# Kernel tuning notes

Hardware: AMD Instinct MI355X
Metric: run time of the kernel (lower is better)

The kernel has to match this reference:

```python
import jax, jax.numpy as jnp
import numpy as np


def setup_inputs() -> dict:
    key = jax.random.key(0)
    kx, ke = jax.random.split(key)
    N, T, D, M = 64, 400, 1024, 256
    x = jax.random.normal(kx, (N, T, D), dtype=jnp.float32)
    embedding = jax.random.normal(ke, (M, D), dtype=jnp.float32)
    return {"x": x, "embedding": embedding}


def reference(x, embedding):
    # x: (N, T, D); embedding (codebook): (M, D)
    M, D = embedding.shape
    # L2_distance: normalize codebook rows, distances to detached x
    emb_norm = embedding / (jnp.linalg.norm(embedding, axis=1, keepdims=True) + 1e-4)
    x_flat = jax.lax.stop_gradient(x).reshape(-1, D)  # (N*T, D)
    distances = (jnp.sum(emb_norm ** 2, axis=1)[None, :]
                 + jnp.sum(x_flat ** 2, axis=1, keepdims=True)
                 - 2.0 * (x_flat @ emb_norm.T))  # (N*T, M)
    indices = jnp.argmin(distances, axis=-1)  # (N*T,)
    encodings = jax.nn.one_hot(indices, M, dtype=jnp.float32)  # (N*T, M)
    quantized = embedding[indices].reshape(x.shape)  # gather from UNnormalized codebook

    # commitment loss (both sides detached in original -> constant)
    commitment_loss = jnp.mean(
        (jax.lax.stop_gradient(x) - jax.lax.stop_gradient(quantized)) ** 2)

    # straight-through + average with quantized
    quantized_st = x + jax.lax.stop_gradient(quantized - x)
    quantized_ = (quantized_st + quantized) / 2.0

    avg_probs = jnp.mean(encodings, axis=0)  # (M,)
    perplexity = jnp.exp(-jnp.sum(avg_probs * jnp.log(avg_probs + 1e-10)))
    return quantized_, commitment_loss, perplexity
```

## Files before the change

### kernel.cpp

```cpp
#include <hip/hip_runtime.h>
#include <cstdint>
#include <cstddef>


typedef __attribute__((ext_vector_type(8))) short short8;
typedef __attribute__((ext_vector_type(4))) float f32x4;

namespace {
constexpr int kNT = 25600;
constexpr int kD  = 1024;
constexpr int kM  = 256;
constexpr size_t kQElems = (size_t)kNT * kD;

constexpr int WS_IMG_H = 0;
constexpr int WS_IMG_L = 131072;
constexpr int WS_E2N   = 262144;
constexpr int WS_SCL   = WS_E2N + kM;
constexpr int WS_E2R   = WS_SCL + kM;
constexpr int WS_COM   = WS_E2R + kM;
constexpr int WS_HIST  = WS_COM + 4;
constexpr int WS_ZERO_BYTES = (WS_HIST + kM - WS_COM) * 4;
}

typedef __attribute__((address_space(3))) unsigned int        lds_u32;
typedef const __attribute__((address_space(1))) unsigned int  glb_u32;
typedef const __attribute__((address_space(3))) char          lds_chc;

__device__ __forceinline__ void gl2lds16(const void* g, void* l) {
  __builtin_amdgcn_global_load_lds((glb_u32*)g, (lds_u32*)l, 16, 0, 0);
}

template <int OFF>
__device__ __forceinline__ short8 ldsr(lds_chc* p) {
  short8 r;
  asm volatile("ds_read_b128 %0, %1 offset:%c2" : "=v"(r) : "v"(p), "i"(OFF));
  return r;
}
template <int OFF>
__device__ __forceinline__ void ldsw(lds_chc* p, short8 v) {
  asm volatile("ds_write_b128 %0, %1 offset:%c2" :: "v"(p), "v"(v), "i"(OFF) : "memory");
}
__device__ __forceinline__ f32x4 gld4(const float* p) {
  f32x4 r;
  asm volatile("global_load_dwordx4 %0, %1, off" : "=v"(r) : "v"(p));
  return r;
}

__global__ __launch_bounds__(256) void vq_normalize(const float* __restrict__ emb,
                                                    float* __restrict__ ws) {
  const int m = blockIdx.x;
  const int t = threadIdx.x;
  const float4 v = reinterpret_cast<const float4*>(emb + (size_t)m * kD)[t];
  float s = v.x * v.x + v.y * v.y + v.z * v.z + v.w * v.w;
#pragma unroll
  for (int mask = 32; mask >= 1; mask >>= 1) s += __shfl_xor(s, mask);
  __shared__ float red[4];
  if ((t & 63) == 0) red[t >> 6] = s;
  __syncthreads();
  const float tot = red[0] + red[1] + red[2] + red[3];
  const float sc  = sqrtf(tot) + 1e-4f;
  const float inv = 1.0f / sc;
  const float4 nv = make_float4(v.x * inv, v.y * inv, v.z * inv, v.w * inv);

  float s2 = nv.x * nv.x + nv.y * nv.y + nv.z * nv.z + nv.w * nv.w;
#pragma unroll
  for (int mask = 32; mask >= 1; mask >>= 1) s2 += __shfl_xor(s2, mask);
  __syncthreads();
  if ((t & 63) == 0) red[t >> 6] = s2;
  __syncthreads();
  if (t == 0) {
    ws[WS_E2N + m] = red[0] + red[1] + red[2] + red[3];
    ws[WS_SCL + m] = sc;
    ws[WS_E2R + m] = tot;
  }

  unsigned short* imgh = (unsigned short*)(ws + WS_IMG_H);
  unsigned short* imgl = (unsigned short*)(ws + WS_IMG_L);
  const int c  = t >> 3;
  const int g  = (t >> 1) & 3;
  const int sq = g ^ ((m >> 1) & 3);
  const int base = c * 8192 + m * 32 + sq * 8 + 4 * (t & 1);
  ushort4 hq, lq;
#pragma unroll
  for (int j = 0; j < 4; ++j) {
    const float fv = (&nv.x)[j];
    const unsigned int b = __float_as_uint(fv);
    const unsigned short hi = (unsigned short)(b >> 16);
    const float lof = fv - __uint_as_float(b & 0xFFFF0000u);
    const unsigned short lo = (unsigned short)(__float_as_uint(lof) >> 16);
    (&hq.x)[j] = hi; (&lq.x)[j] = lo;
  }
  *(ushort4*)(imgh + base) = hq;
  *(ushort4*)(imgl + base) = lq;
}


#define DMASTAGE(KCN)                                                          \
  {                                                                            \
    const unsigned short* gh_ = imgH + ((size_t)(KCN) << 13) + (w << 11) + (l << 3); \
    const unsigned short* gl_ = imgL + ((size_t)(KCN) << 13) + (w << 11) + (l << 3); \
    gl2lds16(gh_,        BslU);                                                \
    gl2lds16(gh_ +  512, BslU + 1024);                                         \
    gl2lds16(gh_ + 1024, BslU + 2048);                                         \
    gl2lds16(gh_ + 1536, BslU + 3072);                                         \
    gl2lds16(gl_,        BslU + 4096);                                         \
    gl2lds16(gl_ +  512, BslU + 5120);                                         \
    gl2lds16(gl_ + 1024, BslU + 6144);                                         \
    gl2lds16(gl_ + 1536, BslU + 7168);                                         \
  }

#define CONV8(F0, F1, AH, AL)                                                  \
  {                                                                            \
    union { short8 v; unsigned short u[8]; } H_, L_;                           \
    _Pragma("unroll")                                                          \
    for (int jj_ = 0; jj_ < 8; ++jj_) {                                        \
      const float fv_ = (jj_ < 4) ? (F0)[jj_] : (F1)[jj_ - 4];                 \
      const unsigned int b_ = __float_as_uint(fv_);                            \
      H_.u[jj_] = (unsigned short)(b_ >> 16);                                  \
      const float lo_ = fv_ - __uint_as_float(b_ & 0xFFFF0000u);               \
      L_.u[jj_] = (unsigned short)(__float_as_uint(lo_) >> 16);                \
      x2 += fv_ * fv_;                                                         \
    }                                                                          \
    AH = H_.v; AL = L_.v;                                                      \
  }

#define MMQ(AR, B0, B1, B2, B3, RT)                                                        \
  acc[RT][0] = __builtin_amdgcn_mfma_f32_16x16x32_bf16(AR, B0, acc[RT][0], 0, 0, 0);       \
  acc[RT][1] = __builtin_amdgcn_mfma_f32_16x16x32_bf16(AR, B1, acc[RT][1], 0, 0, 0);       \
  acc[RT][2] = __builtin_amdgcn_mfma_f32_16x16x32_bf16(AR, B2, acc[RT][2], 0, 0, 0);       \
  acc[RT][3] = __builtin_amdgcn_mfma_f32_16x16x32_bf16(AR, B3, acc[RT][3], 0, 0, 0);
#define MMPASS(A0, A1, A2, A3, B0, B1, B2, B3)                                 \
  MMQ(A0, B0, B1, B2, B3, 0) MMQ(A1, B0, B1, B2, B3, 1)                        \
  MMQ(A2, B0, B1, B2, B3, 2) MMQ(A3, B0, B1, B2, B3, 3)

#define VQ_ITER5(KC, XB, XC0, XC1, XN0, XN1)                                   \
  {                                                                            \
    asm volatile("s_waitcnt vmcnt(2)" ::: "memory");          \
    __builtin_amdgcn_sched_barrier(0);                                         \
    short8 a0h, a1h, a2h, a3h, a0l, a1l, a2l, a3l;                             \
    short8 b0h, b1h, b2h, b3h, b0l, b1l, b2l, b3l;                             \
    a0h = ldsr<32768 + (XB) * 8192 + 0 * 1024>(pA);                            \
    a1h = ldsr<32768 + (XB) * 8192 + 1 * 1024>(pA);                            \
    a2h = ldsr<32768 + (XB) * 8192 + 2 * 1024>(pA);                            \
    a3h = ldsr<32768 + (XB) * 8192 + 3 * 1024>(pA);                            \
    a0l = ldsr<32768 + (XB) * 8192 + 4096 + 0 * 1024>(pA);                     \
    a1l = ldsr<32768 + (XB) * 8192 + 4096 + 1 * 1024>(pA);                     \
    a2l = ldsr<32768 + (XB) * 8192 + 4096 + 2 * 1024>(pA);                     \
    a3l = ldsr<32768 + (XB) * 8192 + 4096 + 3 * 1024>(pA);                     \
    b0h = ldsr<0 * 1024>(pB);                                                  \
    b1h = ldsr<1 * 1024>(pB);                                                  \
    b2h = ldsr<2 * 1024>(pB);                                                  \
    b3h = ldsr<3 * 1024>(pB);                                                  \
    b0l = ldsr<4096 + 0 * 1024>(pB);                                           \
    b1l = ldsr<4096 + 1 * 1024>(pB);                                           \
    b2l = ldsr<4096 + 2 * 1024>(pB);                                           \
    b3l = ldsr<4096 + 3 * 1024>(pB);                                           \
    asm volatile("s_waitcnt lgkmcnt(0)" ::: "memory");      \
    __builtin_amdgcn_sched_barrier(0);                                         \
    {                      \
      const int kcn_ = ((KC) + 1 < 32) ? (KC) + 1 : 31;                        \
      DMASTAGE(kcn_)                                                           \
    }                                                                          \
    {                                                                          \
      const int kc2_ = ((KC) + 2 < 32) ? (KC) + 2 : 31;                        \
      XN0 = gld4(xrow + kc2_ * 32);                                            \
      XN1 = gld4(xrow + kc2_ * 32 + 4);                                        \
    }                                                                          \
    __builtin_amdgcn_s_setprio(1);                                             \
    MMPASS(a0h, a1h, a2h, a3h, b0h, b1h, b2h, b3h)                  \
    MMPASS(a0h, a1h, a2h, a3h, b0l, b1l, b2l, b3l)                  \
    __builtin_amdgcn_s_setprio(0);                                             \
    asm volatile("s_waitcnt vmcnt(10)" ::: "memory");       \
    __builtin_amdgcn_sched_barrier(0);                                         \
    if ((KC) < 31) {                                                           \
      short8 cah, cal;                                                         \
      CONV8(XC0, XC1, cah, cal)                                                \
      ldsw<32768 + ((XB) ^ 1) * 8192 + 0>(pW, cah);                            \
      ldsw<32768 + ((XB) ^ 1) * 8192 + 4096>(pW, cal);                         \
    }                                                                          \
    __builtin_amdgcn_s_setprio(1);                                             \
    MMPASS(a0l, a1l, a2l, a3l, b0h, b1h, b2h, b3h)                  \
    __builtin_amdgcn_s_setprio(0);                                             \
    asm volatile("s_waitcnt lgkmcnt(0)" ::: "memory");      \
    __builtin_amdgcn_s_barrier();                                              \
  }

__global__ __launch_bounds__(256, 2) void vq_main(const float* __restrict__ x,
                                                  const float* __restrict__ emb,
                                                  const float* __restrict__ wsc,
                                                  float* __restrict__ out,
                                                  float* __restrict__ commit_sum,
                                                  int* __restrict__ hist) {
  __shared__ char pool[49152];
  __shared__ float x2s[64];
  __shared__ float bvp[4][64];
  __shared__ int   bjp[4][64];
  __shared__ int   idx_s[64];

  const int t   = threadIdx.x;
  const int l   = t & 63;
  const int w   = t >> 6;
  const int nlo = l & 15;
  const int kq  = l >> 4;
  const int blk0 = blockIdx.x * 64;

  const unsigned short* imgH = (const unsigned short*)(wsc + WS_IMG_H);
  const unsigned short* imgL = (const unsigned short*)(wsc + WS_IMG_L);
  char* BslU = pool + w * 8192;

  const float* xrow = x + (size_t)(blk0 + w * 16 + nlo) * kD + kq * 8;

  const int sqz = kq ^ ((nlo >> 1) & 3);
  lds_chc* base = (lds_chc*)pool;
  lds_chc* pA = base + nlo * 64 + sqz * 16;
  lds_chc* pB = base + w * 8192 + nlo * 64 + sqz * 16;
  lds_chc* pW = pA + w * 1024;

  f32x4 acc[4][4];
#pragma unroll
  for (int i = 0; i < 4; ++i)
#pragma unroll
    for (int j = 0; j < 4; ++j) acc[i][j] = (f32x4)0.0f;
  float x2 = 0.0f;

  f32x4 xa0 = gld4(xrow);
  f32x4 xa1 = gld4(xrow + 4);
  DMASTAGE(0)
  f32x4 xb0 = gld4(xrow + 32);
  f32x4 xb1 = gld4(xrow + 36);
  asm volatile("s_waitcnt vmcnt(10)" ::: "memory");
  __builtin_amdgcn_sched_barrier(0);
  {
    short8 cah, cal;
    CONV8(xa0, xa1, cah, cal)
    ldsw<32768 + 0>(pW, cah);
    ldsw<32768 + 4096>(pW, cal);
  }
  asm volatile("s_waitcnt lgkmcnt(0)" ::: "memory");
  __builtin_amdgcn_s_barrier();

#pragma unroll 1
  for (int kk = 0; kk < 32; kk += 2) {
    VQ_ITER5(kk,     0, xb0, xb1, xa0, xa1)
    VQ_ITER5(kk + 1, 1, xa0, xa1, xb0, xb1)
  }

  asm volatile("s_waitcnt vmcnt(0)"
               :: "v"(xa0), "v"(xa1), "v"(xb0), "v"(xb1) : "memory");

  x2 += __shfl_xor(x2, 16);
  x2 += __shfl_xor(x2, 32);
  if (l < 16) x2s[w * 16 + l] = x2;

  float eN[4];
#pragma unroll
  for (int ct = 0; ct < 4; ++ct) eN[ct] = wsc[WS_E2N + w * 64 + ct * 16 + nlo];

  float bv[4][4]; int bj[4][4];
#pragma unroll
  for (int rt = 0; rt < 4; ++rt)
#pragma unroll
    for (int rg = 0; rg < 4; ++rg) { bv[rt][rg] = 3.0e38f; bj[rt][rg] = 0; }
#pragma unroll
  for (int ct = 0; ct < 4; ++ct) {
    const int j = w * 64 + ct * 16 + nlo;
#pragma unroll
    for (int rt = 0; rt < 4; ++rt)
#pragma unroll
      for (int rg = 0; rg < 4; ++rg) {
        const float v = eN[ct] - 2.0f * acc[rt][ct][rg];
        if (v < bv[rt][rg] || (v == bv[rt][rg] && j < bj[rt][rg])) {
          bv[rt][rg] = v; bj[rt][rg] = j;
        }
      }
  }
#pragma unroll
  for (int mk = 1; mk <= 8; mk <<= 1) {
#pragma unroll
    for (int rt = 0; rt < 4; ++rt)
#pragma unroll
      for (int rg = 0; rg < 4; ++rg) {
        const float ov = __shfl_xor(bv[rt][rg], mk);
        const int   oj = __shfl_xor(bj[rt][rg], mk);
        if (ov < bv[rt][rg] || (ov == bv[rt][rg] && oj < bj[rt][rg])) {
          bv[rt][rg] = ov; bj[rt][rg] = oj;
        }
      }
  }
  if (nlo == 0) {
#pragma unroll
    for (int rt = 0; rt < 4; ++rt)
#pragma unroll
      for (int rg = 0; rg < 4; ++rg) {
        const int row = rt * 16 + kq * 4 + rg;
        bvp[w][row] = bv[rt][rg];
        bjp[w][row] = bj[rt][rg];
      }
  }
  __syncthreads();

  if (t < 64) {
    const int row = t;
    float v = bvp[0][row]; int j = bjp[0][row];
#pragma unroll
    for (int wv = 1; wv < 4; ++wv) {
      const float v2 = bvp[wv][row]; const int j2 = bjp[wv][row];
      if (v2 < v || (v2 == v && j2 < j)) { v = v2; j = j2; }
    }
    idx_s[row] = j;
    atomicAdd(&hist[j], 1);
    float cl = x2s[row] + wsc[WS_E2R + j] - (wsc[WS_E2N + j] - v) * wsc[WS_SCL + j];
#pragma unroll
    for (int mk = 1; mk <= 32; mk <<= 1) cl += __shfl_xor(cl, mk);
    if (t == 0) atomicAdd(commit_sum, cl);
  }
  __syncthreads();

  const float4* emb4 = (const float4*)emb;
  float4* out4 = (float4*)out;
#pragma unroll 2
  for (int rr = 0; rr < 16; ++rr) {
    const int j = idx_s[w * 16 + rr];
    const float4* s = emb4 + (size_t)j * (kD / 4);
    float4* d = out4 + (size_t)(blk0 + w * 16 + rr) * (kD / 4);
#pragma unroll
    for (int c = 0; c < 4; ++c) d[c * 64 + l] = s[c * 64 + l];
  }
}

__global__ __launch_bounds__(256) void vq_final(const int* __restrict__ hist,
                                                const float* __restrict__ commit_sum,
                                                float* __restrict__ out) {
  const int t = threadIdx.x;
  const float p = (float)hist[t] * (1.0f / (float)kNT);
  float s = p * logf(p + 1e-10f);
#pragma unroll
  for (int mask = 32; mask >= 1; mask >>= 1) s += __shfl_xor(s, mask);
  __shared__ float red[4];
  if ((t & 63) == 0) red[t >> 6] = s;
  __syncthreads();
  if (t == 0) {
    const float ent = red[0] + red[1] + red[2] + red[3];
    out[kQElems]     = commit_sum[0] * (1.0f / (float)kQElems);
    out[kQElems + 1] = expf(-ent);
  }
}

extern "C" void kernel_launch(void* const* d_in, const int* in_sizes, int n_in,
                              void* d_out, int out_size, void* d_ws, size_t ws_size,
                              hipStream_t stream) {
  (void)in_sizes; (void)n_in; (void)out_size; (void)ws_size;
  const float* x   = (const float*)d_in[0];
  const float* emb = (const float*)d_in[1];
  float* out = (float*)d_out;
  float* ws  = (float*)d_ws;

  hipMemsetAsync((char*)d_ws + (size_t)WS_COM * 4, 0, WS_ZERO_BYTES, stream);
  hipLaunchKernelGGL(vq_normalize, dim3(kM), dim3(256), 0, stream, emb, ws);
  hipLaunchKernelGGL(vq_main, dim3(kNT / 64), dim3(256), 0, stream,
                     x, emb, ws, out, ws + WS_COM, (int*)(ws + WS_HIST));
  hipLaunchKernelGGL(vq_final, dim3(1), dim3(256), 0, stream,
                     (const int*)(ws + WS_HIST), ws + WS_COM, out);
}
```

Measured before the change: 228.3 us.

## Double-buffer LDS fragments, prefetch next stage, fuse final reduction via ticket

The main GEMM loop is restructured so the LDS fragment reads for the next K-chunk are prefetched into a second register set while the current chunk's MFMAs run. Codebook DMA runs two stages ahead and x loads three ahead, using a larger 80KB LDS pool. The memset and the separate final kernel are removed. Zeroing moves into the normalize kernel, and the perplexity/commitment finalization runs in the last block, chosen by an atomic ticket. This raises register and LDS pressure, which may lower occupancy.

```diff
diff --git a/kernel.cpp b/kernel.cpp
--- a/kernel.cpp
+++ b/kernel.cpp
@@ -19,7 +19,7 @@
 constexpr int WS_E2R   = WS_SCL + kM;
 constexpr int WS_COM   = WS_E2R + kM;
 constexpr int WS_HIST  = WS_COM + 4;
-constexpr int WS_ZERO_BYTES = (WS_HIST + kM - WS_COM) * 4;
+constexpr int WS_TICKET = WS_HIST + kM;
 }
 
 typedef __attribute__((address_space(3))) unsigned int        lds_u32;
@@ -32,12 +32,14 @@
 
 template <int OFF>
 __device__ __forceinline__ short8 ldsr(lds_chc* p) {
+  static_assert(OFF >= 0 && OFF < 65536, "ds offset immediate");
   short8 r;
   asm volatile("ds_read_b128 %0, %1 offset:%c2" : "=v"(r) : "v"(p), "i"(OFF));
   return r;
 }
 template <int OFF>
 __device__ __forceinline__ void ldsw(lds_chc* p, short8 v) {
+  static_assert(OFF >= 0 && OFF < 65536, "ds offset immediate");
   asm volatile("ds_write_b128 %0, %1 offset:%c2" :: "v"(p), "v"(v), "i"(OFF) : "memory");
 }
 __device__ __forceinline__ f32x4 gld4(const float* p) {
@@ -50,6 +52,11 @@
                                                     float* __restrict__ ws) {
   const int m = blockIdx.x;
   const int t = threadIdx.x;
+
+  if (t == 0) ((int*)(ws + WS_HIST))[m] = 0;
+  if (m == 0 && t < 4) ws[WS_COM + t] = 0.0f;
+  if (m == 0 && t == 4) ((int*)(ws + WS_TICKET))[0] = 0;
+
   const float4 v = reinterpret_cast<const float4*>(emb + (size_t)m * kD)[t];
   float s = v.x * v.x + v.y * v.y + v.z * v.z + v.w * v.w;
 #pragma unroll
@@ -95,21 +102,45 @@
 }
 
 
-#define DMASTAGE(KCN)                                                          \
+struct Frags {
+  short8 a0h, a1h, a2h, a3h, a0l, a1l, a2l, a3l;
+  short8 b0h, b1h, b2h, b3h, b0l, b1l, b2l, b3l;
+};
+
+#define DMASTAGE(KCN, P)                                                       \
   {                                                                            \
     const unsigned short* gh_ = imgH + ((size_t)(KCN) << 13) + (w << 11) + (l << 3); \
     const unsigned short* gl_ = imgL + ((size_t)(KCN) << 13) + (w << 11) + (l << 3); \
-    gl2lds16(gh_,        BslU);                                                \
-    gl2lds16(gh_ +  512, BslU + 1024);                                         \
-    gl2lds16(gh_ + 1024, BslU + 2048);                                         \
-    gl2lds16(gh_ + 1536, BslU + 3072);                                         \
-    gl2lds16(gl_,        BslU + 4096);                                         \
-    gl2lds16(gl_ +  512, BslU + 5120);                                         \
-    gl2lds16(gl_ + 1024, BslU + 6144);                                         \
-    gl2lds16(gl_ + 1536, BslU + 7168);                                         \
-  }
-
-#define CONV8(F0, F1, AH, AL)                                                  \
+    char* dg_ = pool + 16384 + (P) * 32768 + w * 8192;                         \
+    gl2lds16(gh_,        dg_);                                                 \
+    gl2lds16(gh_ +  512, dg_ + 1024);                                          \
+    gl2lds16(gh_ + 1024, dg_ + 2048);                                          \
+    gl2lds16(gh_ + 1536, dg_ + 3072);                                          \
+    gl2lds16(gl_,        dg_ + 4096);                                          \
+    gl2lds16(gl_ +  512, dg_ + 5120);                                          \
+    gl2lds16(gl_ + 1024, dg_ + 6144);                                          \
+    gl2lds16(gl_ + 1536, dg_ + 7168);                                          \
+  }
+
+#define PREFETCH(PN, FN)                                                       \
+  (FN).b0h = ldsr<16384 + (PN) * 32768 + 0 * 1024>(pB);                        \
+  (FN).b1h = ldsr<16384 + (PN) * 32768 + 1 * 1024>(pB);                        \
+  (FN).b2h = ldsr<16384 + (PN) * 32768 + 2 * 1024>(pB);                        \
+  (FN).b3h = ldsr<16384 + (PN) * 32768 + 3 * 1024>(pB);                        \
+  (FN).b0l = ldsr<16384 + (PN) * 32768 + 4096 + 0 * 1024>(pB);                 \
+  (FN).b1l = ldsr<16384 + (PN) * 32768 + 4096 + 1 * 1024>(pB);                 \
+  (FN).b2l = ldsr<16384 + (PN) * 32768 + 4096 + 2 * 1024>(pB);                 \
+  (FN).b3l = ldsr<16384 + (PN) * 32768 + 4096 + 3 * 1024>(pB);                 \
+  (FN).a0h = ldsr<(PN) * 8192 + 0 * 1024>(pA);                                 \
+  (FN).a1h = ldsr<(PN) * 8192 + 1 * 1024>(pA);                                 \
+  (FN).a2h = ldsr<(PN) * 8192 + 2 * 1024>(pA);                                 \
+  (FN).a3h = ldsr<(PN) * 8192 + 3 * 1024>(pA);                                 \
+  (FN).a0l = ldsr<(PN) * 8192 + 4096 + 0 * 1024>(pA);                          \
+  (FN).a1l = ldsr<(PN) * 8192 + 4096 + 1 * 1024>(pA);                         \
+  (FN).a2l = ldsr<(PN) * 8192 + 4096 + 2 * 1024>(pA);                          \
+  (FN).a3l = ldsr<(PN) * 8192 + 4096 + 3 * 1024>(pA);
+
+#define CONV8(F0, F1, AH, AL, X2EN)                                            \
   {                                                                            \
     union { short8 v; unsigned short u[8]; } H_, L_;                           \
     _Pragma("unroll")                                                          \
@@ -119,7 +150,7 @@
       H_.u[jj_] = (unsigned short)(b_ >> 16);                                  \
       const float lo_ = fv_ - __uint_as_float(b_ & 0xFFFF0000u);               \
       L_.u[jj_] = (unsigned short)(__float_as_uint(lo_) >> 16);                \
-      x2 += fv_ * fv_;                                                         \
+      if (X2EN) x2 += fv_ * fv_;                                               \
     }                                                                          \
     AH = H_.v; AL = L_.v;                                                      \
   }
@@ -133,55 +164,37 @@
   MMQ(A0, B0, B1, B2, B3, 0) MMQ(A1, B0, B1, B2, B3, 1)                        \
   MMQ(A2, B0, B1, B2, B3, 2) MMQ(A3, B0, B1, B2, B3, 3)
 
-#define VQ_ITER5(KC, XB, XC0, XC1, XN0, XN1)                                   \
+#define VQ_ITER7(KC, P, FC, FN, XC0, XC1, XN0, XN1)                            \
   {                                                                            \
-    asm volatile("s_waitcnt vmcnt(2)" ::: "memory");          \
+    __builtin_amdgcn_s_setprio(1);                                             \
+    MMPASS(FC.a0h, FC.a1h, FC.a2h, FC.a3h, FC.b0h, FC.b1h, FC.b2h, FC.b3h)     \
+    __builtin_amdgcn_s_setprio(0);                                             \
+    asm volatile("s_waitcnt vmcnt(8)" ::: "memory");       \
     __builtin_amdgcn_sched_barrier(0);                                         \
-    short8 a0h, a1h, a2h, a3h, a0l, a1l, a2l, a3l;                             \
-    short8 b0h, b1h, b2h, b3h, b0l, b1l, b2l, b3l;                             \
-    a0h = ldsr<32768 + (XB) * 8192 + 0 * 1024>(pA);                            \
-    a1h = ldsr<32768 + (XB) * 8192 + 1 * 1024>(pA);                            \
-    a2h = ldsr<32768 + (XB) * 8192 + 2 * 1024>(pA);                            \
-    a3h = ldsr<32768 + (XB) * 8192 + 3 * 1024>(pA);                            \
-    a0l = ldsr<32768 + (XB) * 8192 + 4096 + 0 * 1024>(pA);                     \
-    a1l = ldsr<32768 + (XB) * 8192 + 4096 + 1 * 1024>(pA);                     \
-    a2l = ldsr<32768 + (XB) * 8192 + 4096 + 2 * 1024>(pA);                     \
-    a3l = ldsr<32768 + (XB) * 8192 + 4096 + 3 * 1024>(pA);                     \
-    b0h = ldsr<0 * 1024>(pB);                                                  \
-    b1h = ldsr<1 * 1024>(pB);                                                  \
-    b2h = ldsr<2 * 1024>(pB);                                                  \
-    b3h = ldsr<3 * 1024>(pB);                                                  \
-    b0l = ldsr<4096 + 0 * 1024>(pB);                                           \
-    b1l = ldsr<4096 + 1 * 1024>(pB);                                           \
-    b2l = ldsr<4096 + 2 * 1024>(pB);                                           \
-    b3l = ldsr<4096 + 3 * 1024>(pB);                                           \
-    asm volatile("s_waitcnt lgkmcnt(0)" ::: "memory");      \
-    __builtin_amdgcn_sched_barrier(0);                                         \
-    {                      \
-      const int kcn_ = ((KC) + 1 < 32) ? (KC) + 1 : 31;                        \
-      DMASTAGE(kcn_)                                                           \
+    if ((KC) < 30) {                                                           \
+      short8 cah, cal;                                                         \
+      CONV8(XC0, XC1, cah, cal, 1)                                             \
+      ldsw<(P) * 8192 + 0>(pW, cah);                                           \
+      ldsw<(P) * 8192 + 4096>(pW, cal);                                        \
     }                                                                          \
     {                                                                          \
-      const int kc2_ = ((KC) + 2 < 32) ? (KC) + 2 : 31;                        \
-      XN0 = gld4(xrow + kc2_ * 32);                                            \
-      XN1 = gld4(xrow + kc2_ * 32 + 4);                                        \
+      const int kx_ = ((KC) + 3 < 32) ? (KC) + 3 : 31;                         \
+      XN0 = gld4(xrow + kx_ * 32);                                             \
+      XN1 = gld4(xrow + kx_ * 32 + 4);                                         \
+      const int kb_ = ((KC) + 2 < 32) ? (KC) + 2 : 31;                         \
+      DMASTAGE(kb_, P)                                                         \
     }                                                                          \
     __builtin_amdgcn_s_setprio(1);                                             \
-    MMPASS(a0h, a1h, a2h, a3h, b0h, b1h, b2h, b3h)                  \
-    MMPASS(a0h, a1h, a2h, a3h, b0l, b1l, b2l, b3l)                  \
+    MMPASS(FC.a0h, FC.a1h, FC.a2h, FC.a3h, FC.b0l, FC.b1l, FC.b2l, FC.b3l)     \
     __builtin_amdgcn_s_setprio(0);                                             \
-    asm volatile("s_waitcnt vmcnt(10)" ::: "memory");       \
+    asm volatile("s_waitcnt vmcnt(10)" ::: "memory");      \
     __builtin_amdgcn_sched_barrier(0);                                         \
-    if ((KC) < 31) {                                                           \
-      short8 cah, cal;                                                         \
-      CONV8(XC0, XC1, cah, cal)                                                \
-      ldsw<32768 + ((XB) ^ 1) * 8192 + 0>(pW, cah);                            \
-      ldsw<32768 + ((XB) ^ 1) * 8192 + 4096>(pW, cal);                         \
-    }                                                                          \
+    PREFETCH((P) ^ 1, FN)                                                      \
     __builtin_amdgcn_s_setprio(1);                                             \
-    MMPASS(a0l, a1l, a2l, a3l, b0h, b1h, b2h, b3h)                  \
+    MMPASS(FC.a0l, FC.a1l, FC.a2l, FC.a3l, FC.b0h, FC.b1h, FC.b2h, FC.b3h)     \
     __builtin_amdgcn_s_setprio(0);                                             \
-    asm volatile("s_waitcnt lgkmcnt(0)" ::: "memory");      \
+    asm volatile("s_waitcnt lgkmcnt(0)" ::: "memory");  \
+    __builtin_amdgcn_sched_barrier(0);                                         \
     __builtin_amdgcn_s_barrier();                                              \
   }
 
@@ -190,12 +203,9 @@
                                                   const float* __restrict__ wsc,
                                                   float* __restrict__ out,
                                                   float* __restrict__ commit_sum,
-                                                  int* __restrict__ hist) {
-  __shared__ char pool[49152];
-  __shared__ float x2s[64];
-  __shared__ float bvp[4][64];
-  __shared__ int   bjp[4][64];
-  __shared__ int   idx_s[64];
+                                                  int* __restrict__ hist,
+                                                  int* __restrict__ ticket) {
+  __shared__ char pool[81920];
 
   const int t   = threadIdx.x;
   const int l   = t & 63;
@@ -206,7 +216,6 @@
 
   const unsigned short* imgH = (const unsigned short*)(wsc + WS_IMG_H);
   const unsigned short* imgL = (const unsigned short*)(wsc + WS_IMG_L);
-  char* BslU = pool + w * 8192;
 
   const float* xrow = x + (size_t)(blk0 + w * 16 + nlo) * kD + kq * 8;
 
@@ -223,30 +232,54 @@
     for (int j = 0; j < 4; ++j) acc[i][j] = (f32x4)0.0f;
   float x2 = 0.0f;
 
+  Frags F0, F1;
+
   f32x4 xa0 = gld4(xrow);
   f32x4 xa1 = gld4(xrow + 4);
-  DMASTAGE(0)
   f32x4 xb0 = gld4(xrow + 32);
   f32x4 xb1 = gld4(xrow + 36);
+  DMASTAGE(0, 0)
   asm volatile("s_waitcnt vmcnt(10)" ::: "memory");
   __builtin_amdgcn_sched_barrier(0);
   {
     short8 cah, cal;
-    CONV8(xa0, xa1, cah, cal)
-    ldsw<32768 + 0>(pW, cah);
-    ldsw<32768 + 4096>(pW, cal);
-  }
+    CONV8(xa0, xa1, cah, cal, 1)
+    ldsw<0>(pW, cah);
+    ldsw<4096>(pW, cal);
+  }
+  asm volatile("s_waitcnt vmcnt(8)" ::: "memory");
+  __builtin_amdgcn_sched_barrier(0);
+  {
+    short8 cah, cal;
+    CONV8(xb0, xb1, cah, cal, 1)
+    ldsw<8192 + 0>(pW, cah);
+    ldsw<8192 + 4096>(pW, cal);
+  }
+  xa0 = gld4(xrow + 2 * 32);
+  xa1 = gld4(xrow + 2 * 32 + 4);
+  DMASTAGE(1, 1)
   asm volatile("s_waitcnt lgkmcnt(0)" ::: "memory");
+  __builtin_amdgcn_sched_barrier(0);
   __builtin_amdgcn_s_barrier();
+  asm volatile("s_waitcnt vmcnt(10)" ::: "memory");
+  __builtin_amdgcn_sched_barrier(0);
+  PREFETCH(0, F0)
+  asm volatile("s_waitcnt lgkmcnt(0)" ::: "memory");
+  __builtin_amdgcn_sched_barrier(0);
 
 #pragma unroll 1
   for (int kk = 0; kk < 32; kk += 2) {
-    VQ_ITER5(kk,     0, xb0, xb1, xa0, xa1)
-    VQ_ITER5(kk + 1, 1, xa0, xa1, xb0, xb1)
+    VQ_ITER7(kk,     0, F0, F1, xa0, xa1, xb0, xb1)
+    VQ_ITER7(kk + 1, 1, F1, F0, xb0, xb1, xa0, xa1)
   }
 
   asm volatile("s_waitcnt vmcnt(0)"
                :: "v"(xa0), "v"(xa1), "v"(xb0), "v"(xb1) : "memory");
+
+  float* x2s  = (float*)pool;
+  float* bvp  = x2s + 64;
+  int*   bjp  = (int*)(bvp + 256);
+  int*   idxs = bjp + 256;
 
   x2 += __shfl_xor(x2, 16);
   x2 += __shfl_xor(x2, 32);
@@ -287,27 +320,28 @@
         }
       }
   }
+  __syncthreads();
   if (nlo == 0) {
 #pragma unroll
     for (int rt = 0; rt < 4; ++rt)
 #pragma unroll
       for (int rg = 0; rg < 4; ++rg) {
         const int row = rt * 16 + kq * 4 + rg;
-        bvp[w][row] = bv[rt][rg];
-        bjp[w][row] = bj[rt][rg];
+        bvp[w * 64 + row] = bv[rt][rg];
+        bjp[w * 64 + row] = bj[rt][rg];
       }
   }
   __syncthreads();
 
   if (t < 64) {
     const int row = t;
-    float v = bvp[0][row]; int j = bjp[0][row];
+    float v = bvp[row]; int j = bjp[row];
 #pragma unroll
     for (int wv = 1; wv < 4; ++wv) {
-      const float v2 = bvp[wv][row]; const int j2 = bjp[wv][row];
+      const float v2 = bvp[wv * 64 + row]; const int j2 = bjp[wv * 64 + row];
       if (v2 < v || (v2 == v && j2 < j)) { v = v2; j = j2; }
     }
-    idx_s[row] = j;
+    idxs[row] = j;
     atomicAdd(&hist[j], 1);
     float cl = x2s[row] + wsc[WS_E2R + j] - (wsc[WS_E2N + j] - v) * wsc[WS_SCL + j];
 #pragma unroll
@@ -320,29 +354,32 @@
   float4* out4 = (float4*)out;
 #pragma unroll 2
   for (int rr = 0; rr < 16; ++rr) {
-    const int j = idx_s[w * 16 + rr];
+    const int j = idxs[w * 16 + rr];
     const float4* s = emb4 + (size_t)j * (kD / 4);
     float4* d = out4 + (size_t)(blk0 + w * 16 + rr) * (kD / 4);
 #pragma unroll
     for (int c = 0; c < 4; ++c) d[c * 64 + l] = s[c * 64 + l];
   }
-}
-
-__global__ __launch_bounds__(256) void vq_final(const int* __restrict__ hist,
-                                                const float* __restrict__ commit_sum,
-                                                float* __restrict__ out) {
-  const int t = threadIdx.x;
-  const float p = (float)hist[t] * (1.0f / (float)kNT);
-  float s = p * logf(p + 1e-10f);
-#pragma unroll
-  for (int mask = 32; mask >= 1; mask >>= 1) s += __shfl_xor(s, mask);
-  __shared__ float red[4];
-  if ((t & 63) == 0) red[t >> 6] = s;
-  __syncthreads();
-  if (t == 0) {
-    const float ent = red[0] + red[1] + red[2] + red[3];
-    out[kQElems]     = commit_sum[0] * (1.0f / (float)kQElems);
-    out[kQElems + 1] = expf(-ent);
+
+  __threadfence();
+  int* doneflag = (int*)(pool + 4160);
+  if (t == 0) *doneflag = atomicAdd(ticket, 1);
+  __syncthreads();
+  if (*doneflag == (kNT / 64) - 1) {
+    const int h = atomicAdd(&hist[t], 0);
+    const float p = (float)h * (1.0f / (float)kNT);
+    float s = p * logf(p + 1e-10f);
+#pragma unroll
+    for (int mask = 32; mask >= 1; mask >>= 1) s += __shfl_xor(s, mask);
+    float* red = (float*)(pool + 4096);
+    if ((t & 63) == 0) red[t >> 6] = s;
+    __syncthreads();
+    if (t == 0) {
+      const float ent = red[0] + red[1] + red[2] + red[3];
+      const float cs = atomicAdd(commit_sum, 0.0f);
+      out[kQElems]     = cs * (1.0f / (float)kQElems);
+      out[kQElems + 1] = expf(-ent);
+    }
   }
 }
 
@@ -355,10 +392,8 @@
   float* out = (float*)d_out;
   float* ws  = (float*)d_ws;
 
-  hipMemsetAsync((char*)d_ws + (size_t)WS_COM * 4, 0, WS_ZERO_BYTES, stream);
   hipLaunchKernelGGL(vq_normalize, dim3(kM), dim3(256), 0, stream, emb, ws);
   hipLaunchKernelGGL(vq_main, dim3(kNT / 64), dim3(256), 0, stream,
-                     x, emb, ws, out, ws + WS_COM, (int*)(ws + WS_HIST));
-  hipLaunchKernelGGL(vq_final, dim3(1), dim3(256), 0, stream,
-                     (const int*)(ws + WS_HIST), ws + WS_COM, out);
-}
+                     x, emb, ws, out, ws + WS_COM, (int*)(ws + WS_HIST),
+                     (int*)(ws + WS_TICKET));
+}
```

After: 300.6 us. 1.32x slower.
